# Performance work log

Measured on AMD Instinct MI355X. Metric: run time of the kernel, lower is better.

The kernel has to match this reference:

```python
import jax, jax.numpy as jnp
import numpy as np

N_NODES = 50000
N_EDGES = 1600000
D_IN = 64
D_HID = 64
N_CLASSES = 10
N_GRAPHS = 64


def setup_inputs() -> dict:
    key = jax.random.key(0)
    ks = jax.random.split(key, 9)
    x = jax.random.normal(ks[0], (N_NODES, D_IN), dtype=jnp.float32)
    edge_index = jax.random.randint(ks[1], (2, N_EDGES), 0, N_NODES, dtype=jnp.int64)
    batch = jnp.sort(jax.random.randint(ks[2], (N_NODES,), 0, N_GRAPHS, dtype=jnp.int64))
    s1 = 1.0 / np.sqrt(D_IN)
    s2 = 1.0 / np.sqrt(D_HID)
    W1 = jax.random.uniform(ks[3], (D_IN, D_HID), jnp.float32, -s1, s1)
    b1 = jnp.zeros((D_HID,), jnp.float32)
    W2 = jax.random.uniform(ks[4], (D_HID, D_HID), jnp.float32, -s2, s2)
    b2 = jnp.zeros((D_HID,), jnp.float32)
    Wfc = jax.random.uniform(ks[5], (D_HID, N_CLASSES), jnp.float32, -s2, s2)
    bfc = jnp.zeros((N_CLASSES,), jnp.float32)
    return {"x": x, "edge_index": edge_index, "batch": batch,
            "W1": W1, "b1": b1, "W2": W2, "b2": b2, "Wfc": Wfc, "bfc": bfc}


def _gcn_conv(h, src, dst, deg_inv_sqrt, W, b):
    # h: [N, d_in] -> linear then normalized scatter-add aggregation (PyG GCNConv)
    h = h @ W                                   # [N, d_out]
    norm = deg_inv_sqrt[src] * deg_inv_sqrt[dst]  # [E+N]
    msg = h[src] * norm[:, None]                # gather + scale  [E+N, d_out]
    out = jax.ops.segment_sum(msg, dst, num_segments=h.shape[0])
    return out + b


def reference(x, edge_index, batch, W1, b1, W2, b2, Wfc, bfc):
    n = x.shape[0]
    loops = jnp.arange(n, dtype=edge_index.dtype)
    src = jnp.concatenate([edge_index[0], loops])  # self-loops appended
    dst = jnp.concatenate([edge_index[1], loops])
    deg = jax.ops.segment_sum(jnp.ones_like(dst, x.dtype), dst, num_segments=n)
    deg_inv_sqrt = jnp.where(deg > 0, jax.lax.rsqrt(deg), 0.0)

    h = jax.nn.relu(_gcn_conv(x, src, dst, deg_inv_sqrt, W1, b1))
    # dropout is identity in eval mode
    h = jax.nn.relu(_gcn_conv(h, src, dst, deg_inv_sqrt, W2, b2))

    # global mean pool over graphs
    sums = jax.ops.segment_sum(h, batch, num_segments=N_GRAPHS)      # [G, d]
    cnts = jax.ops.segment_sum(jnp.ones((n,), h.dtype), batch, num_segments=N_GRAPHS)
    pooled = sums / jnp.maximum(cnts, 1.0)[:, None]
    return pooled @ Wfc + bfc                                        # [G, classes]
```

## Files before the change

kernel.cpp:

```cpp
#include <hip/hip_runtime.h>
#include <hip/hip_bf16.h>

#define THREADS 256
#define PART_T 8192
#define NF_PAD 1024
#define BCAP 2560
#define CAPN 80

__device__ __forceinline__ bool detect_f64_block(const unsigned* __restrict__ raw,
                                                 int nelem, int* nz, int t) {
    if (t == 0) *nz = 0;
    __syncthreads();
    int found = 0;
    int lim = nelem < 2048 ? nelem : 2048;
#pragma unroll
    for (int k = 0; k < 8; k++) {
        int i = t * 8 + k;
        if (i < lim) found |= (raw[2 * i + 1] != 0u);
    }
    if (found) atomicOr(nz, 1);
    __syncthreads();
    return (*nz) == 0;
}

__device__ __forceinline__ float bf_lo(unsigned u) { return __uint_as_float(u << 16); }
__device__ __forceinline__ float bf_hi(unsigned u) { return __uint_as_float(u & 0xFFFF0000u); }
__device__ __forceinline__ unsigned short f2bf(float f) {
    __hip_bfloat16 h = __float2bfloat16(f);
    unsigned short u;
    __builtin_memcpy(&u, &h, 2);
    return u;
}
__device__ __forceinline__ unsigned pack2bf(float a, float b) {
    return (unsigned)f2bf(a) | ((unsigned)f2bf(b) << 16);
}

__global__ __launch_bounds__(256) void partition_edges(const int* __restrict__ raw, int E,
                                                       int NF, int* __restrict__ gcur,
                                                       unsigned* __restrict__ elist) {
    __shared__ int cnt[NF_PAD];
    __shared__ int pfx[NF_PAD];
    __shared__ int gbase[NF_PAD];
    __shared__ int tsum[256];
    __shared__ unsigned stage[PART_T];
    __shared__ int nz;
    int t = threadIdx.x;
    bool f64 = detect_f64_block((const unsigned*)raw, 2 * E, &nz, t);
    long long base = (long long)blockIdx.x * PART_T;
    int tileN = (int)min((long long)PART_T, (long long)E - base);

    for (int i = t; i < NF_PAD; i += 256) cnt[i] = 0;
    __syncthreads();

    unsigned pk[PART_T / 256];
#pragma unroll
    for (int k = 0; k < PART_T / 256; k++) {
        long long e = base + k * 256 + t;
        if (e < (long long)E) {
            int s = f64 ? raw[2 * e] : raw[e];
            int d = f64 ? raw[2 * ((long long)E + e)] : raw[E + e];
            unsigned p = (unsigned)s | ((unsigned)d << 16);
            pk[k] = p;
            atomicAdd(&cnt[d >> 6], 1);
        } else {
            pk[k] = 0xFFFFFFFFu;
        }
    }
    __syncthreads();

    int a0 = cnt[4 * t], a1 = cnt[4 * t + 1], a2 = cnt[4 * t + 2], a3 = cnt[4 * t + 3];
    int tot = a0 + a1 + a2 + a3;
    tsum[t] = tot;
    __syncthreads();
    for (int o = 1; o < 256; o <<= 1) {
        int x = (t >= o) ? tsum[t - o] : 0;
        __syncthreads();
        tsum[t] += x;
        __syncthreads();
    }
    int pre = tsum[t] - tot;
    pfx[4 * t] = pre;
    pfx[4 * t + 1] = pre + a0;
    pfx[4 * t + 2] = pre + a0 + a1;
    pfx[4 * t + 3] = pre + a0 + a1 + a2;

    for (int i = t; i < NF; i += 256) {
        gbase[i] = (cnt[i] > 0) ? (i * BCAP + atomicAdd(&gcur[i], cnt[i])) : 0;
    }
    __syncthreads();
    for (int i = t; i < NF_PAD; i += 256) cnt[i] = 0;
    __syncthreads();

#pragma unroll
    for (int k = 0; k < PART_T / 256; k++) {
        long long e = base + k * 256 + t;
        if (e < (long long)E) {
            unsigned p = pk[k];
            int f = p >> 22;
            int r = atomicAdd(&cnt[f], 1);
            stage[pfx[f] + r] = p;
        }
    }
    __syncthreads();

    for (int i = t; i < tileN; i += 256) {
        unsigned v = stage[i];
        int f = v >> 22;
        elist[gbase[f] + (i - pfx[f])] = v;
    }
}

__global__ __launch_bounds__(256) void bucket_csr(const unsigned* __restrict__ elist,
                                                  const int* __restrict__ gcur,
                                                  int n,
                                                  unsigned short* __restrict__ ssrc,
                                                  int* __restrict__ deg,
                                                  float* __restrict__ dis) {
    __shared__ int cnt[64];
    int b = blockIdx.x;
    int t = threadIdx.x;
    int beg = b * BCAP, end = beg + gcur[b];
    if (t < 64) cnt[t] = 0;
    __syncthreads();
    for (int e = beg + t; e < end; e += 256) {
        unsigned v = elist[e];
        int local = (v >> 16) & 63;
        int r = atomicAdd(&cnt[local], 1);
        if (r < CAPN)
            ssrc[(long long)(b * 64 + local) * CAPN + r] = (unsigned short)(v & 0xFFFFu);
    }
    __syncthreads();
    if (t < 64) {
        int node = b * 64 + t;
        if (node < n) {
            int d = cnt[t];
            deg[node] = d;
            dis[node] = rsqrtf((float)(d + 1));
        }
    }
}

__global__ __launch_bounds__(256) void linear64_f32(const float* __restrict__ in,
                                                    const float* __restrict__ W,
                                                    const float* __restrict__ dis,
                                                    __hip_bfloat16* __restrict__ outH, int n) {
    __shared__ float sIn[64][64];
    int t = threadIdx.x;
    int ln = t >> 6, od = t & 63;
    float w[64];
#pragma unroll
    for (int k = 0; k < 64; k++) w[k] = W[k * 64 + od];
    int base = blockIdx.x * 64;
    long long ebase = (long long)base * 64;
    long long etot = (long long)n * 64;
#pragma unroll
    for (int pass = 0; pass < 16; pass++) {
        long long idx = ebase + pass * 256 + t;
        sIn[(pass * 256 + t) >> 6][(pass * 256 + t) & 63] = (idx < etot) ? in[idx] : 0.f;
    }
    __syncthreads();
    for (int pass = 0; pass < 16; pass++) {
        int node = base + pass * 4 + ln;
        if (node < n) {
            float acc = 0.f;
#pragma unroll
            for (int k = 0; k < 64; k++) acc += sIn[pass * 4 + ln][k] * w[k];
            outH[(long long)node * 64 + od] = __float2bfloat16(acc * dis[node]);
        }
    }
}

__global__ __launch_bounds__(256) void linear64_bf16(const unsigned short* __restrict__ inH,
                                                     const float* __restrict__ W,
                                                     const float* __restrict__ dis,
                                                     __hip_bfloat16* __restrict__ outH, int n) {
    __shared__ float sIn[64][64];
    int t = threadIdx.x;
    int ln = t >> 6, od = t & 63;
    float w[64];
#pragma unroll
    for (int k = 0; k < 64; k++) w[k] = W[k * 64 + od];
    int base = blockIdx.x * 64;
    long long ebase2 = (long long)base * 32;
    long long etot2 = ((long long)n * 64) >> 1;
#pragma unroll
    for (int pass = 0; pass < 8; pass++) {
        int li = pass * 256 + t;
        long long idx = ebase2 + li;
        unsigned u = (idx < etot2) ? ((const unsigned*)inH)[idx] : 0u;
        sIn[(2 * li) >> 6][(2 * li) & 63] = bf_lo(u);
        sIn[(2 * li) >> 6][(2 * li + 1) & 63] = bf_hi(u);
    }
    __syncthreads();
    for (int pass = 0; pass < 16; pass++) {
        int node = base + pass * 4 + ln;
        if (node < n) {
            float acc = 0.f;
#pragma unroll
            for (int k = 0; k < 64; k++) acc += sIn[pass * 4 + ln][k] * w[k];
            outH[(long long)node * 64 + od] = __float2bfloat16(acc * dis[node]);
        }
    }
}

__global__ __launch_bounds__(256) void gather_agg(const unsigned short* __restrict__ hs,
                                                  const int* __restrict__ deg,
                                                  const unsigned short* __restrict__ ssrc,
                                                  const float* __restrict__ dis,
                                                  const float* __restrict__ bias,
                                                  __hip_bfloat16* __restrict__ outH, int n) {
    int t = threadIdx.x;
    int lane = t & 63;
    int g = lane >> 3;
    int l = lane & 7;
    int node = blockIdx.x * 4 + (t >> 6);
    if (node >= n) return;
    long long beg = (long long)node * CAPN;
    int d = deg[node];
    float a0 = 0.f, a1 = 0.f, a2 = 0.f, a3 = 0.f, a4 = 0.f, a5 = 0.f, a6 = 0.f, a7 = 0.f;

    if (d <= 32) {
        int idx[4];
#pragma unroll
        for (int k = 0; k < 4; k++) idx[k] = (int)ssrc[beg + g + 8 * k];
#pragma unroll
        for (int k = 0; k < 4; k++) {
            uint4 v = ((const uint4*)(hs + (long long)idx[k] * 64))[l];
            if (g + 8 * k >= d) { v.x = 0u; v.y = 0u; v.z = 0u; v.w = 0u; }
            a0 += bf_lo(v.x); a1 += bf_hi(v.x);
            a2 += bf_lo(v.y); a3 += bf_hi(v.y);
            a4 += bf_lo(v.z); a5 += bf_hi(v.z);
            a6 += bf_lo(v.w); a7 += bf_hi(v.w);
        }
    } else {
        int idx[8];
#pragma unroll
        for (int k = 0; k < 8; k++) idx[k] = (int)ssrc[beg + g + 8 * k];
#pragma unroll
        for (int k = 0; k < 8; k++) {
            uint4 v = ((const uint4*)(hs + (long long)idx[k] * 64))[l];
            if (g + 8 * k >= d) { v.x = 0u; v.y = 0u; v.z = 0u; v.w = 0u; }
            a0 += bf_lo(v.x); a1 += bf_hi(v.x);
            a2 += bf_lo(v.y); a3 += bf_hi(v.y);
            a4 += bf_lo(v.z); a5 += bf_hi(v.z);
            a6 += bf_lo(v.w); a7 += bf_hi(v.w);
        }
        for (int i = 64 + g; i < d; i += 8) {
            int s = (int)ssrc[beg + i];
            uint4 v = ((const uint4*)(hs + (long long)s * 64))[l];
            a0 += bf_lo(v.x); a1 += bf_hi(v.x);
            a2 += bf_lo(v.y); a3 += bf_hi(v.y);
            a4 += bf_lo(v.z); a5 += bf_hi(v.z);
            a6 += bf_lo(v.w); a7 += bf_hi(v.w);
        }
    }
    if (g == 0) {
        uint4 v = ((const uint4*)(hs + (long long)node * 64))[l];
        a0 += bf_lo(v.x); a1 += bf_hi(v.x);
        a2 += bf_lo(v.y); a3 += bf_hi(v.y);
        a4 += bf_lo(v.z); a5 += bf_hi(v.z);
        a6 += bf_lo(v.w); a7 += bf_hi(v.w);
    }
#pragma unroll
    for (int o = 8; o <= 32; o <<= 1) {
        a0 += __shfl_xor(a0, o, 64);
        a1 += __shfl_xor(a1, o, 64);
        a2 += __shfl_xor(a2, o, 64);
        a3 += __shfl_xor(a3, o, 64);
        a4 += __shfl_xor(a4, o, 64);
        a5 += __shfl_xor(a5, o, 64);
        a6 += __shfl_xor(a6, o, 64);
        a7 += __shfl_xor(a7, o, 64);
    }
    if (g == 0) {
        float dv = dis[node];
        const float4* bp = (const float4*)bias;
        float4 b0 = bp[2 * l], b1 = bp[2 * l + 1];
        float r0 = dv * a0 + b0.x; r0 = r0 > 0.f ? r0 : 0.f;
        float r1 = dv * a1 + b0.y; r1 = r1 > 0.f ? r1 : 0.f;
        float r2 = dv * a2 + b0.z; r2 = r2 > 0.f ? r2 : 0.f;
        float r3 = dv * a3 + b0.w; r3 = r3 > 0.f ? r3 : 0.f;
        float r4 = dv * a4 + b1.x; r4 = r4 > 0.f ? r4 : 0.f;
        float r5 = dv * a5 + b1.y; r5 = r5 > 0.f ? r5 : 0.f;
        float r6 = dv * a6 + b1.z; r6 = r6 > 0.f ? r6 : 0.f;
        float r7 = dv * a7 + b1.w; r7 = r7 > 0.f ? r7 : 0.f;
        uint4 o4;
        o4.x = pack2bf(r0, r1);
        o4.y = pack2bf(r2, r3);
        o4.z = pack2bf(r4, r5);
        o4.w = pack2bf(r6, r7);
        ((uint4*)(outH + (long long)node * 64))[l] = o4;
    }
}

__global__ __launch_bounds__(256) void pool_fc(const unsigned short* __restrict__ h2,
                                               const int* __restrict__ braw, int n,
                                               const float* __restrict__ Wfc,
                                               const float* __restrict__ bfc,
                                               float* __restrict__ out) {
    __shared__ int nz;
    __shared__ float sred[256];
    __shared__ float pooled[64];
    int t = threadIdx.x;
    int gph = blockIdx.x;
    bool f64 = detect_f64_block((const unsigned*)braw, n, &nz, t);

    int lo = 0, hi = n;
    while (lo < hi) {
        int m = (lo + hi) >> 1;
        int v = f64 ? braw[2 * m] : braw[m];
        if (v < gph) lo = m + 1; else hi = m;
    }
    int lo2 = lo, hi2 = n;
    while (lo2 < hi2) {
        int m = (lo2 + hi2) >> 1;
        int v = f64 ? braw[2 * m] : braw[m];
        if (v < gph + 1) lo2 = m + 1; else hi2 = m;
    }
    int cnt = lo2 - lo;

    int col = t & 63, rg = t >> 6;
    float acc = 0.f;
    for (int r = lo + rg; r < lo2; r += 4) {
        unsigned short u = h2[(long long)r * 64 + col];
        acc += __uint_as_float((unsigned)u << 16);
    }
    sred[t] = acc;
    __syncthreads();
    if (t < 64) {
        float s = sred[t] + sred[t + 64] + sred[t + 128] + sred[t + 192];
        float c = (float)cnt;
        if (c < 1.f) c = 1.f;
        pooled[t] = s / c;
    }
    __syncthreads();
    if (t < 10) {
        float acc2 = 0.f;
#pragma unroll
        for (int k = 0; k < 64; k++) acc2 += pooled[k] * Wfc[k * 10 + t];
        out[gph * 10 + t] = acc2 + bfc[t];
    }
}

static inline int cdiv(long long a, int b) { return (int)((a + b - 1) / b); }

extern "C" void kernel_launch(void* const* d_in, const int* in_sizes, int n_in,
                              void* d_out, int out_size, void* d_ws, size_t ws_size,
                              hipStream_t stream) {
    const float* x    = (const float*)d_in[0];
    const int*   eraw = (const int*)d_in[1];
    const int*   braw = (const int*)d_in[2];
    const float* W1   = (const float*)d_in[3];
    const float* b1   = (const float*)d_in[4];
    const float* W2   = (const float*)d_in[5];
    const float* b2   = (const float*)d_in[6];
    const float* Wfc  = (const float*)d_in[7];
    const float* bfc  = (const float*)d_in[8];
    float* out = (float*)d_out;

    const int N  = in_sizes[0] / 64;
    const int E  = in_sizes[1] / 2;
    const int NF = cdiv(N, 64);

    char* p = (char*)d_ws;
    auto carve = [&](size_t bytes) { char* q = p; p += (bytes + 255) / 256 * 256; return q; };
    unsigned*       elist = (unsigned*)carve(((size_t)NF + 1) * BCAP * sizeof(unsigned));
    unsigned short* ssrc  = (unsigned short*)carve((size_t)(NF + 1) * 64 * CAPN * sizeof(unsigned short));
    int*            gcur  = (int*)carve((size_t)NF * sizeof(int));
    int*            deg   = (int*)carve((size_t)N * sizeof(int));
    float*          dis   = (float*)carve((size_t)N * sizeof(float));
    __hip_bfloat16* hs    = (__hip_bfloat16*)carve((size_t)N * 64 * sizeof(__hip_bfloat16));
    __hip_bfloat16* h1    = (__hip_bfloat16*)carve((size_t)N * 64 * sizeof(__hip_bfloat16));
    __hip_bfloat16* h2    = (__hip_bfloat16*)carve((size_t)N * 64 * sizeof(__hip_bfloat16));
    (void)carve(4 << 20);

    hipMemsetAsync(gcur, 0, (size_t)NF * sizeof(int), stream);

    partition_edges<<<cdiv(E, PART_T), 256, 0, stream>>>(eraw, E, NF, gcur, elist);
    bucket_csr<<<NF, 256, 0, stream>>>(elist, gcur, N, ssrc, deg, dis);

    linear64_f32<<<cdiv(N, 64), 256, 0, stream>>>(x, W1, dis, hs, N);
    gather_agg<<<cdiv(N, 4), 256, 0, stream>>>((const unsigned short*)hs, deg, ssrc, dis, b1, h1, N);

    linear64_bf16<<<cdiv(N, 64), 256, 0, stream>>>((const unsigned short*)h1, W2, dis, hs, N);
    gather_agg<<<cdiv(N, 4), 256, 0, stream>>>((const unsigned short*)hs, deg, ssrc, dis, b2, h2, N);

    pool_fc<<<64, 256, 0, stream>>>((const unsigned short*)h2, braw, N, Wfc, bfc, out);
}
```

Measured before the change: 261.8 us.

## Split graph pooling into parallel atomic partial sums plus tiny FC kernel

Replaces the 64-block pool_fc, which used one block per graph and serially walked about 780 nodes per graph, with pool_sum launched over about 391 blocks. Each wavefront handles 32 consecutive nodes and atomically adds per-graph partial sums and counts. A separate single-block final_fc then divides by the counts and applies the FC layer. The aim is to spread the pooling read of h2 across many more CUs, at the cost of one more kernel launch, global float atomics (summation order no longer fixed), and extra zeroed workspace.

Result: faster. 228.9 us (-12.6%).

```diff
diff --git a/kernel.cpp b/kernel.cpp
--- a/kernel.cpp
+++ b/kernel.cpp
@@ -293,53 +293,56 @@
     }
 }
 
-__global__ __launch_bounds__(256) void pool_fc(const unsigned short* __restrict__ h2,
-                                               const int* __restrict__ braw, int n,
-                                               const float* __restrict__ Wfc,
-                                               const float* __restrict__ bfc,
-                                               float* __restrict__ out) {
+__global__ __launch_bounds__(256) void pool_sum(const unsigned short* __restrict__ h2,
+                                                const int* __restrict__ braw,
+                                                float* __restrict__ psum,
+                                                int* __restrict__ pcnt, int n) {
     __shared__ int nz;
-    __shared__ float sred[256];
-    __shared__ float pooled[64];
-    int t = threadIdx.x;
-    int gph = blockIdx.x;
+    int t = threadIdx.x;
     bool f64 = detect_f64_block((const unsigned*)braw, n, &nz, t);
-
-    int lo = 0, hi = n;
-    while (lo < hi) {
-        int m = (lo + hi) >> 1;
-        int v = f64 ? braw[2 * m] : braw[m];
-        if (v < gph) lo = m + 1; else hi = m;
-    }
-    int lo2 = lo, hi2 = n;
-    while (lo2 < hi2) {
-        int m = (lo2 + hi2) >> 1;
-        int v = f64 ? braw[2 * m] : braw[m];
-        if (v < gph + 1) lo2 = m + 1; else hi2 = m;
-    }
-    int cnt = lo2 - lo;
-
-    int col = t & 63, rg = t >> 6;
+    int lane = t & 63;
+    int base = (blockIdx.x * 4 + (t >> 6)) * 32;
     float acc = 0.f;
-    for (int r = lo + rg; r < lo2; r += 4) {
-        unsigned short u = h2[(long long)r * 64 + col];
+    int g = -1, cnt = 0;
+    for (int i = 0; i < 32; i++) {
+        int node = base + i;
+        if (node >= n) break;
+        int bg = f64 ? braw[2 * node] : braw[node];
+        if (bg != g) {
+            if (g >= 0) {
+                atomicAdd(&psum[g * 64 + lane], acc);
+                if (lane == 0) atomicAdd(&pcnt[g], cnt);
+            }
+            g = bg; acc = 0.f; cnt = 0;
+        }
+        unsigned short u = h2[(long long)node * 64 + lane];
         acc += __uint_as_float((unsigned)u << 16);
-    }
-    sred[t] = acc;
-    __syncthreads();
-    if (t < 64) {
-        float s = sred[t] + sred[t + 64] + sred[t + 128] + sred[t + 192];
-        float c = (float)cnt;
-        if (c < 1.f) c = 1.f;
-        pooled[t] = s / c;
-    }
-    __syncthreads();
-    if (t < 10) {
-        float acc2 = 0.f;
-#pragma unroll
-        for (int k = 0; k < 64; k++) acc2 += pooled[k] * Wfc[k * 10 + t];
-        out[gph * 10 + t] = acc2 + bfc[t];
-    }
+        cnt++;
+    }
+    if (g >= 0) {
+        atomicAdd(&psum[g * 64 + lane], acc);
+        if (lane == 0) atomicAdd(&pcnt[g], cnt);
+    }
+}
+
+__global__ __launch_bounds__(640) void final_fc(const float* __restrict__ psum,
+                                                const int* __restrict__ pcnt,
+                                                const float* __restrict__ Wfc,
+                                                const float* __restrict__ bfc,
+                                                float* __restrict__ out) {
+    __shared__ float sP[64 * 64];
+    __shared__ float sW[64 * 10];
+    int t = threadIdx.x;
+    for (int i = t; i < 4096; i += 640) sP[i] = psum[i];
+    if (t < 640) sW[t] = Wfc[t];
+    __syncthreads();
+    int g = t / 10, c = t % 10;
+    float acc = 0.f;
+#pragma unroll
+    for (int k = 0; k < 64; k++) acc += sP[g * 64 + k] * sW[k * 10 + c];
+    float cnt = (float)pcnt[g];
+    if (cnt < 1.f) cnt = 1.f;
+    out[g * 10 + c] = acc / cnt + bfc[c];
 }
 
 static inline int cdiv(long long a, int b) { return (int)((a + b - 1) / b); }
@@ -366,7 +369,11 @@
     auto carve = [&](size_t bytes) { char* q = p; p += (bytes + 255) / 256 * 256; return q; };
     unsigned*       elist = (unsigned*)carve(((size_t)NF + 1) * BCAP * sizeof(unsigned));
     unsigned short* ssrc  = (unsigned short*)carve((size_t)(NF + 1) * 64 * CAPN * sizeof(unsigned short));
+    char* zbeg = p;
     int*            gcur  = (int*)carve((size_t)NF * sizeof(int));
+    float*          psum  = (float*)carve(64 * 64 * sizeof(float));
+    int*            pcnt  = (int*)carve(64 * sizeof(int));
+    size_t zlen = (size_t)(p - zbeg);
     int*            deg   = (int*)carve((size_t)N * sizeof(int));
     float*          dis   = (float*)carve((size_t)N * sizeof(float));
     __hip_bfloat16* hs    = (__hip_bfloat16*)carve((size_t)N * 64 * sizeof(__hip_bfloat16));
@@ -374,7 +381,7 @@
     __hip_bfloat16* h2    = (__hip_bfloat16*)carve((size_t)N * 64 * sizeof(__hip_bfloat16));
     (void)carve(4 << 20);
 
-    hipMemsetAsync(gcur, 0, (size_t)NF * sizeof(int), stream);
+    hipMemsetAsync(zbeg, 0, zlen, stream);
 
     partition_edges<<<cdiv(E, PART_T), 256, 0, stream>>>(eraw, E, NF, gcur, elist);
     bucket_csr<<<NF, 256, 0, stream>>>(elist, gcur, N, ssrc, deg, dis);
@@ -385,5 +392,6 @@
     linear64_bf16<<<cdiv(N, 64), 256, 0, stream>>>((const unsigned short*)h1, W2, dis, hs, N);
     gather_agg<<<cdiv(N, 4), 256, 0, stream>>>((const unsigned short*)hs, deg, ssrc, dis, b2, h2, N);
 
-    pool_fc<<<64, 256, 0, stream>>>((const unsigned short*)h2, braw, N, Wfc, bfc, out);
-}
+    pool_sum<<<cdiv(N, 128), 256, 0, stream>>>((const unsigned short*)h2, braw, psum, pcnt, N);
+    final_fc<<<1, 640, 0, stream>>>(psum, pcnt, Wfc, bfc, out);
+}
```
